# Kernel tuning notes

Hardware: AMD Instinct MI355X
Metric: run time of the kernel (lower is better)

## Reference

```python
import jax, jax.numpy as jnp
from jax import lax
import numpy as np

DIM = 768
HEADS = 8
DH = DIM // HEADS          # 96
M = DIM // 2               # 384 landmarks
PINV_ITERS = 6
RES_K = 33                 # residual depthwise conv kernel
EPS_LN = 1e-5


def layernorm(x, w, b):
    mu = jnp.mean(x, axis=-1, keepdims=True)
    var = jnp.mean((x - mu) ** 2, axis=-1, keepdims=True)
    return (x - mu) * lax.rsqrt(var + EPS_LN) * w + b


def conv1d_same(x, w, b):
    # x: [B, C, N], w: [O, I, K]
    k = w.shape[-1]
    y = lax.conv_general_dilated(x, w, (1,), [(k // 2, k // 2)],
                                 dimension_numbers=('NCH', 'OIH', 'NCH'))
    return y + b[None, :, None]


def moore_penrose_pinv(x, iters=PINV_ITERS):
    # x: [..., m, m]
    abs_x = jnp.abs(x)
    col = jnp.max(abs_x.sum(axis=-1))
    row = jnp.max(abs_x.sum(axis=-2))
    z = jnp.swapaxes(x, -1, -2) / (col * row)
    I = jnp.eye(x.shape[-1], dtype=x.dtype)
    for _ in range(iters):
        xz = x @ z
        z = 0.25 * z @ (13 * I - xz @ (15 * I - xz @ (7 * I - xz)))
    return z


def nystrom_attention(x, qkv_w, out_w, out_b, res_conv_w):
    # x: [B, N, DIM]; N divisible by M here, so no padding branch.
    b, n, _ = x.shape
    qkv = x @ qkv_w.T                                   # [B, N, 3*DIM]
    q, k, v = jnp.split(qkv, 3, axis=-1)
    def heads(t):
        return t.reshape(b, n, HEADS, DH).transpose(0, 2, 1, 3)  # [B,H,N,Dh]
    q, k, v = heads(q), heads(k), heads(v)
    q = q * (DH ** -0.5)

    l = n // M
    q_l = q.reshape(b, HEADS, M, l, DH).mean(axis=3)    # [B,H,M,Dh]
    k_l = k.reshape(b, HEADS, M, l, DH).mean(axis=3)

    sim1 = jnp.einsum('bhnd,bhmd->bhnm', q, k_l)        # [B,H,N,M]
    sim2 = jnp.einsum('bhid,bhjd->bhij', q_l, k_l)      # [B,H,M,M]
    sim3 = jnp.einsum('bhmd,bhnd->bhmn', q_l, k)        # [B,H,M,N]
    attn1 = jax.nn.softmax(sim1, axis=-1)
    attn2 = jax.nn.softmax(sim2, axis=-1)
    attn3 = jax.nn.softmax(sim3, axis=-1)

    attn2_inv = moore_penrose_pinv(attn2)
    out = attn1 @ (attn2_inv @ (attn3 @ v))             # [B,H,N,Dh]

    # residual depthwise conv along sequence, per head: kernel (33,1), groups=HEADS
    res = lax.conv_general_dilated(v, res_conv_w, (1, 1),
                                   [(RES_K // 2, RES_K // 2), (0, 0)],
                                   dimension_numbers=('NCHW', 'OIHW', 'NCHW'),
                                   feature_group_count=HEADS)
    out = out + res
    out = out.transpose(0, 2, 1, 3).reshape(b, n, DIM)
    return out @ out_w.T + out_b


def setup_inputs() -> dict:
    key = jax.random.key(0)
    ks = jax.random.split(key, 16)
    B, N = 2, 3840
    s = 0.02
    return {
        'x': jax.random.normal(ks[0], (B, N, DIM), jnp.float32),
        'conv1_w': jax.random.normal(ks[1], (DIM, DIM, 3), jnp.float32) * s,
        'conv1_b': jnp.zeros((DIM,), jnp.float32),
        'conv2_w': jax.random.normal(ks[2], (DIM, DIM, 5), jnp.float32) * s,
        'conv2_b': jnp.zeros((DIM,), jnp.float32),
        'conv3_w': jax.random.normal(ks[3], (DIM, DIM, 7), jnp.float32) * s,
        'conv3_b': jnp.zeros((DIM,), jnp.float32),
        'norm_w': jnp.ones((DIM,), jnp.float32),
        'norm_b': jnp.zeros((DIM,), jnp.float32),
        'tnorm_w': jnp.ones((DIM,), jnp.float32),
        'tnorm_b': jnp.zeros((DIM,), jnp.float32),
        'qkv_w': jax.random.normal(ks[4], (3 * DIM, DIM), jnp.float32) * s,
        'out_w': jax.random.normal(ks[5], (DIM, DIM), jnp.float32) * s,
        'out_b': jnp.zeros((DIM,), jnp.float32),
        'res_conv_w': jax.random.normal(ks[6], (HEADS, 1, RES_K, 1), jnp.float32) * s,
    }


def reference(x, conv1_w, conv1_b, conv2_w, conv2_b, conv3_w, conv3_b,
              norm_w, norm_b, tnorm_w, tnorm_b, qkv_w, out_w, out_b, res_conv_w):
    inp = x.transpose(0, 2, 1)                              # [B, C, N]
    o1 = jax.nn.relu(layernorm(conv1d_same(inp, conv1_w, conv1_b).transpose(0, 2, 1), norm_w, norm_b))
    o2 = jax.nn.relu(layernorm(conv1d_same(inp, conv2_w, conv2_b).transpose(0, 2, 1), norm_w, norm_b))
    o3 = jax.nn.relu(layernorm(conv1d_same(inp, conv3_w, conv3_b).transpose(0, 2, 1), norm_w, norm_b))
    out = o1 + o2 + o3 + x
    # TransLayer: x + attn(norm(x))  (dropout is identity at inference)
    out = out + nystrom_attention(layernorm(out, tnorm_w, tnorm_b),
                                  qkv_w, out_w, out_b, res_conv_w)
    return layernorm(out, norm_w, norm_b)
```

## Files before the change

### kernel.cpp

```cpp
#include <hip/hip_runtime.h>

#define SEQN 3840
#define BATCH 2
#define DIMC 768
#define NH 8
#define DHD 96
#define ML 384
#define LW 10
#define BHN 16
#define ROWS (BATCH*SEQN)
#define PADX 4
#define XPADN (SEQN + 2*PADX)
#define NCOL3 (3*DIMC)
#define KD7 (7*DIMC)

static const int BND = BATCH*SEQN*DIMC;
static const int MD  = BHN*ML*DHD;
static const int MM_ = BHN*ML*ML;

__device__ __forceinline__ unsigned short f2bf(float f) {
    unsigned int u = __float_as_uint(f);
    u = (u + 0x7FFF + ((u >> 16) & 1)) >> 16;
    return (unsigned short)u;
}
__device__ __forceinline__ float bf2f(unsigned short s) {
    return __uint_as_float(((unsigned int)s) << 16);
}
__device__ __forceinline__ unsigned short f2h(float f) {
    _Float16 h = (_Float16)f;
    return *(unsigned short*)&h;
}
__device__ __forceinline__ float h2f(unsigned short u) {
    _Float16 h = *(_Float16*)&u;
    return (float)h;
}

__device__ __forceinline__ float wave_sum(float v) {
#pragma unroll
    for (int m = 32; m; m >>= 1) v += __shfl_xor(v, m, 64);
    return v;
}
__device__ __forceinline__ float wave_max(float v) {
#pragma unroll
    for (int m = 32; m; m >>= 1) v = fmaxf(v, __shfl_xor(v, m, 64));
    return v;
}

typedef short bf16x8 __attribute__((ext_vector_type(8)));
typedef float f32x4 __attribute__((ext_vector_type(4)));
#define ROWP 40

__global__ __launch_bounds__(256) void mgemm_k(
    const unsigned short* __restrict__ A, int lda, long long sA,
    const unsigned short* __restrict__ Bm, int ldb, long long sB,
    int Mr, int Nc, int Kd, float alpha, int conv_k,
    int epi, float* __restrict__ Cf, long long sC, int ldc,
    unsigned short* __restrict__ Cb, const float* __restrict__ bias,
    unsigned short* __restrict__ Qo, unsigned short* __restrict__ Ko,
    unsigned short* __restrict__ Vo)
{
    __shared__ unsigned short As[128*ROWP] __attribute__((aligned(16)));
    __shared__ unsigned short Bs[128*ROWP] __attribute__((aligned(16)));
    const int bz = blockIdx.z;
    const long long aoff = (long long)bz * sA, boff = (long long)bz * sB;
    const long long coff = (long long)bz * sC;
    const int i0 = blockIdx.y * 128, j0 = blockIdx.x * 128;
    const int tid = threadIdx.x;
    const int w = tid >> 6, l = tid & 63;
    const int wr = (w >> 1) << 6, wc = (w & 1) << 6;
    const int lr = l & 15, lk = l >> 4;
    const int khalf = conv_k >> 1;

    f32x4 acc[4][4] = {};

    for (int k0 = 0; k0 < Kd; k0 += 32) {
#pragma unroll
        for (int pass = 0; pass < 2; ++pass) {
            const int flat = tid + pass * 256;
            const int row = flat >> 2, seg = (flat & 3) << 3;
            long long ga;
            if (conv_k) {
                const int gi = i0 + row;
                const int b = gi / SEQN, n = gi - b * SEQN;
                const int tap = k0 / DIMC, c = k0 - tap * DIMC;
                ga = ((long long)(b * XPADN + n + tap + PADX - khalf)) * DIMC + c + seg;
            } else {
                ga = aoff + (long long)(i0 + row) * lda + k0 + seg;
            }
            *(uint4*)&As[row * ROWP + seg] = *(const uint4*)&A[ga];
        }
#pragma unroll
        for (int pass = 0; pass < 2; ++pass) {
            const int flat = tid + pass * 256;
            const int row = flat >> 2, seg = (flat & 3) << 3;
            const int gj = j0 + row;
            uint4 v;
            if (gj < Nc) v = *(const uint4*)&Bm[boff + (long long)gj * ldb + k0 + seg];
            else { v.x = v.y = v.z = v.w = 0u; }
            *(uint4*)&Bs[row * ROWP + seg] = v;
        }
        __syncthreads();
        bf16x8 af[4], bfv[4];
#pragma unroll
        for (int fi = 0; fi < 4; ++fi)
            af[fi] = *(const bf16x8*)&As[(wr + fi * 16 + lr) * ROWP + lk * 8];
#pragma unroll
        for (int fj = 0; fj < 4; ++fj)
            bfv[fj] = *(const bf16x8*)&Bs[(wc + fj * 16 + lr) * ROWP + lk * 8];
#pragma unroll
        for (int fi = 0; fi < 4; ++fi)
#pragma unroll
            for (int fj = 0; fj < 4; ++fj)
                acc[fi][fj] = __builtin_amdgcn_mfma_f32_16x16x32_bf16(
                    af[fi], bfv[fj], acc[fi][fj], 0, 0, 0);
        __syncthreads();
    }
#pragma unroll
    for (int fi = 0; fi < 4; ++fi) {
#pragma unroll
        for (int fj = 0; fj < 4; ++fj) {
            const int col = j0 + wc + fj * 16 + lr;
            if (col >= Nc) continue;
#pragma unroll
            for (int r = 0; r < 4; ++r) {
                const int row = i0 + wr + fi * 16 + lk * 4 + r;
                float v = acc[fi][fj][r] * alpha;
                if (epi == 0) {
                    Cf[coff + (long long)row * ldc + col] = v;
                } else if (epi == 1) {
                    const long long ix = coff + (long long)row * ldc + col;
                    Cf[ix] = Cf[ix] + v + bias[col];
                } else if (epi == 4) {
                    Cb[coff + (long long)row * ldc + col] = f2h(v);
                } else {
                    const int which = col / DIMC;
                    const int c = col - which * DIMC;
                    const int h = c / DHD, d = c - h * DHD;
                    const int b = row / SEQN, n = row - b * SEQN;
                    const long long o = (((long long)(b * NH + h)) * SEQN + n) * DHD + d;
                    if (which == 0)      Qo[o] = f2bf(v * 0.10206207261596575f);
                    else if (which == 1) Ko[o] = f2bf(v);
                    else                 Vo[o] = f2bf(v);
                }
            }
        }
    }
}

template<int BMODE>
__global__ __launch_bounds__(256) void mgemm64_k(
    const unsigned short* __restrict__ A, int lda, long long sA,
    const unsigned short* __restrict__ Bm, int ldb, long long sB,
    int Mr, int Nc, int Kd, float alpha, int bdiag, float bda, int ksplit,
    int epi, float* __restrict__ Cf, long long sC, int ldc,
    unsigned short* __restrict__ Cb)
{
    __shared__ unsigned short As[64*ROWP] __attribute__((aligned(16)));
    __shared__ unsigned short Bs[64*ROWP] __attribute__((aligned(16)));
    const int bz = blockIdx.z / ksplit;
    const int kch = blockIdx.z - bz * ksplit;
    const long long aoff = (long long)bz * sA, boff = (long long)bz * sB;
    const long long coff = (long long)bz * sC;
    const int i0 = blockIdx.y * 64, j0 = blockIdx.x * 64;
    const int tid = threadIdx.x;
    const int w = tid >> 6, l = tid & 63;
    const int lr = l & 15, lk = l >> 4;
    const int klen = Kd / ksplit;
    const int kbeg = kch * klen, kend = kbeg + klen;

    f32x4 acc[4] = {};

    for (int k0 = kbeg; k0 < kend; k0 += 32) {
        {
            const int row = tid >> 2, seg = (tid & 3) << 3;
            *(uint4*)&As[row*ROWP+seg] =
                *(const uint4*)&A[aoff + (long long)(i0+row)*lda + k0 + seg];
        }
        if (BMODE == 0) {
            const int row = tid >> 2, seg = (tid & 3) << 3;
            const int gj = j0 + row;
            uint4 v;
            if (gj < Nc) v = *(const uint4*)&Bm[boff + (long long)gj*ldb + k0 + seg];
            else { v.x=v.y=v.z=v.w=0u; }
            *(uint4*)&Bs[row*ROWP+seg] = v;
        } else {
            const int kk = tid >> 3, j8 = (tid & 7) << 3;
            const int gk = k0 + kk, gj0 = j0 + j8;
            unsigned short buf[8];
            if (gj0 + 8 <= Nc) {
                *(uint4*)&buf[0] = *(const uint4*)&Bm[boff + (long long)gk*ldb + gj0];
                if (bdiag) {
#pragma unroll
                    for (int u = 0; u < 8; ++u) {
                        float v = ((gk == gj0+u) ? bda : 0.f) - bf2f(buf[u]);
                        buf[u] = f2bf(v);
                    }
                }
            } else {
#pragma unroll
                for (int u = 0; u < 8; ++u) buf[u] = 0;
            }
#pragma unroll
            for (int u = 0; u < 8; ++u) Bs[(j8+u)*ROWP + kk] = buf[u];
        }
        __syncthreads();
        bf16x8 af = *(const bf16x8*)&As[(w*16+lr)*ROWP + lk*8];
        bf16x8 b0 = *(const bf16x8*)&Bs[(lr)*ROWP + lk*8];
        bf16x8 b1 = *(const bf16x8*)&Bs[(16+lr)*ROWP + lk*8];
        bf16x8 b2 = *(const bf16x8*)&Bs[(32+lr)*ROWP + lk*8];
        bf16x8 b3 = *(const bf16x8*)&Bs[(48+lr)*ROWP + lk*8];
        acc[0] = __builtin_amdgcn_mfma_f32_16x16x32_bf16(af, b0, acc[0], 0,0,0);
        acc[1] = __builtin_amdgcn_mfma_f32_16x16x32_bf16(af, b1, acc[1], 0,0,0);
        acc[2] = __builtin_amdgcn_mfma_f32_16x16x32_bf16(af, b2, acc[2], 0,0,0);
        acc[3] = __builtin_amdgcn_mfma_f32_16x16x32_bf16(af, b3, acc[3], 0,0,0);
        __syncthreads();
    }
#pragma unroll
    for (int fj = 0; fj < 4; ++fj) {
        const int col = j0 + fj*16 + lr;
        if (col >= Nc) continue;
#pragma unroll
        for (int r = 0; r < 4; ++r) {
            const int row = i0 + w*16 + lk*4 + r;
            float v = acc[fj][r] * alpha;
            if (epi == 0)      Cf[coff + (long long)row*ldc + col] = v;
            else if (epi == 2) Cb[coff + (long long)row*ldc + col] = f2bf(v);
            else               atomicAdd(&Cf[coff + (long long)row*ldc + col], v);
        }
    }
}

template<int NV>
__global__ __launch_bounds__(256) void softmax_h2b(unsigned short* __restrict__ data, int W)
{
    __shared__ float red[4];
    const long long r = blockIdx.x;
    unsigned short* row = data + r * (long long)W;
    const int t = threadIdx.x, lane = t & 63, wid = t >> 6;
    float v[NV];
    float mx = -3.4e38f;
#pragma unroll
    for (int i = 0; i < NV; ++i) {
        const int j = t + i * 256;
        float f = -3.4e38f;
        if (j < W) f = h2f(row[j]);
        v[i] = f;
        mx = fmaxf(mx, f);
    }
    mx = wave_max(mx);
    if (lane == 0) red[wid] = mx;
    __syncthreads();
    mx = fmaxf(fmaxf(red[0], red[1]), fmaxf(red[2], red[3]));
    __syncthreads();
    float s = 0.f;
#pragma unroll
    for (int i = 0; i < NV; ++i) {
        v[i] = __expf(v[i] - mx);
        s += v[i];
    }
    s = wave_sum(s);
    if (lane == 0) red[wid] = s;
    __syncthreads();
    s = red[0] + red[1] + red[2] + red[3];
    const float inv = 1.f / s;
#pragma unroll
    for (int i = 0; i < NV; ++i) {
        const int j = t + i * 256;
        if (j < W) row[j] = f2bf(v[i] * inv);
    }
}

__global__ __launch_bounds__(256) void ln_kernel(
    const float* __restrict__ in, const float* __restrict__ w,
    const float* __restrict__ b, float* __restrict__ outf,
    unsigned short* __restrict__ outb)
{
    __shared__ float red[4];
    const long long r = blockIdx.x;
    const float* row = in + r * DIMC;
    const int t = threadIdx.x, lane = t & 63, wid = t >> 6;
    float x0 = row[t], x1 = row[t+256], x2 = row[t+512];
    float s = wave_sum(x0 + x1 + x2);
    if (lane == 0) red[wid] = s;
    __syncthreads();
    float mu = (red[0]+red[1]+red[2]+red[3]) * (1.f/DIMC);
    __syncthreads();
    float d0 = x0-mu, d1 = x1-mu, d2 = x2-mu;
    float q = wave_sum(d0*d0 + d1*d1 + d2*d2);
    if (lane == 0) red[wid] = q;
    __syncthreads();
    float rs = rsqrtf((red[0]+red[1]+red[2]+red[3]) * (1.f/DIMC) + 1e-5f);
    float v0 = d0*rs*w[t]     + b[t];
    float v1 = d1*rs*w[t+256] + b[t+256];
    float v2 = d2*rs*w[t+512] + b[t+512];
    if (outf) {
        float* o = outf + r * DIMC;
        o[t] = v0; o[t+256] = v1; o[t+512] = v2;
    }
    if (outb) {
        unsigned short* o = outb + r * DIMC;
        o[t] = f2bf(v0); o[t+256] = f2bf(v1); o[t+512] = f2bf(v2);
    }
}

__global__ __launch_bounds__(256) void ln_relu_add3_kernel(
    const unsigned short* __restrict__ Y16,
    const float* __restrict__ cb0, const float* __restrict__ cb1,
    const float* __restrict__ cb2,
    const float* __restrict__ w, const float* __restrict__ b,
    const float* __restrict__ xin, float* __restrict__ acc)
{
    __shared__ float red[4];
    const long long r = blockIdx.x;
    const unsigned short* row = Y16 + r * NCOL3;
    const int t = threadIdx.x, lane = t & 63, wid = t >> 6;
    const float* xr = xin + r * DIMC;
    float o0 = xr[t], o1 = xr[t+256], o2 = xr[t+512];
    const float* cbs[3] = {cb0, cb1, cb2};
#pragma unroll
    for (int s = 0; s < 3; ++s) {
        const float* cb = cbs[s];
        float x0 = h2f(row[s*DIMC + t])     + cb[t];
        float x1 = h2f(row[s*DIMC + t+256]) + cb[t+256];
        float x2 = h2f(row[s*DIMC + t+512]) + cb[t+512];
        float su = wave_sum(x0 + x1 + x2);
        __syncthreads();
        if (lane == 0) red[wid] = su;
        __syncthreads();
        float mu = (red[0]+red[1]+red[2]+red[3]) * (1.f/DIMC);
        float d0 = x0-mu, d1 = x1-mu, d2 = x2-mu;
        float q = wave_sum(d0*d0 + d1*d1 + d2*d2);
        __syncthreads();
        if (lane == 0) red[wid] = q;
        __syncthreads();
        float rs = rsqrtf((red[0]+red[1]+red[2]+red[3]) * (1.f/DIMC) + 1e-5f);
        o0 += fmaxf(d0*rs*w[t]     + b[t],     0.f);
        o1 += fmaxf(d1*rs*w[t+256] + b[t+256], 0.f);
        o2 += fmaxf(d2*rs*w[t+512] + b[t+512], 0.f);
    }
    float* ar = acc + r * DIMC;
    ar[t] = o0; ar[t+256] = o1; ar[t+512] = o2;
}

__global__ __launch_bounds__(256) void softmax_rows(float* __restrict__ data, int W)
{
    __shared__ float red[4];
    const long long r = blockIdx.x;
    float* row = data + r * (long long)W;
    const int t = threadIdx.x, lane = t & 63, wid = t >> 6;
    float mx = -3.4e38f;
    for (int j = t; j < W; j += 256) mx = fmaxf(mx, row[j]);
    mx = wave_max(mx);
    if (lane == 0) red[wid] = mx;
    __syncthreads();
    mx = fmaxf(fmaxf(red[0], red[1]), fmaxf(red[2], red[3]));
    __syncthreads();
    float s = 0.f;
    for (int j = t; j < W; j += 256) s += __expf(row[j] - mx);
    s = wave_sum(s);
    if (lane == 0) red[wid] = s;
    __syncthreads();
    s = red[0]+red[1]+red[2]+red[3];
    const float inv = 1.f / s;
    for (int j = t; j < W; j += 256) row[j] = __expf(row[j] - mx) * inv;
}

__global__ void pad_x_kernel(const float* __restrict__ x, unsigned short* __restrict__ xp)
{
    int i = blockIdx.x * 256 + threadIdx.x;
    if (i >= BATCH * XPADN * (DIMC/4)) return;
    int e = i * 4;
    int c = e % DIMC; int rr = e / DIMC; int pr = rr % XPADN; int b = rr / XPADN;
    int n = pr - PADX;
    ushort4 o;
    if (n < 0 || n >= SEQN) { o.x = o.y = o.z = o.w = 0; }
    else {
        float4 v = *(const float4*)&x[((long long)(b * SEQN + n)) * DIMC + c];
        o.x = f2bf(v.x); o.y = f2bf(v.y); o.z = f2bf(v.z); o.w = f2bf(v.w);
    }
    *(ushort4*)&xp[e] = o;
}

__global__ void transpose_w7_kernel(const float* __restrict__ W,
                                    unsigned short* __restrict__ WT, int K, int branch)
{
    int idx = blockIdx.x * 256 + threadIdx.x;
    if (idx >= DIMC * 7 * DIMC) return;
    int i = idx % DIMC; int rem = idx / DIMC; int t = rem % 7; int o = rem / 7;
    int k = t - (3 - (K >> 1));
    float v = (k >= 0 && k < K) ? W[((long long)o * DIMC + i) * K + k] : 0.f;
    WT[((long long)(branch * DIMC + o)) * KD7 + t * DIMC + i] = f2bf(v);
}

__global__ void cvt_bf16_kernel(const float* __restrict__ src,
                                unsigned short* __restrict__ dst, int n4)
{
    int i = blockIdx.x * 256 + threadIdx.x;
    if (i >= n4) return;
    float4 v = ((const float4*)src)[i];
    ushort4 o; o.x = f2bf(v.x); o.y = f2bf(v.y); o.z = f2bf(v.z); o.w = f2bf(v.w);
    ((ushort4*)dst)[i] = o;
}

__global__ void zero_f32_kernel(float* __restrict__ p, int n)
{
    int i = blockIdx.x * 256 + threadIdx.x;
    if (i < n) p[i] = 0.f;
}

__global__ void landmark_kernel(const unsigned short* __restrict__ src,
                                unsigned short* __restrict__ dstb)
{
    int idx = blockIdx.x * 256 + threadIdx.x;
    if (idx >= MD) return;
    int d = idx % DHD; int rem = idx / DHD; int m = rem % ML; int bh = rem / ML;
    const unsigned short* p = src + ((long long)bh * SEQN + m * LW) * DHD + d;
    float s = 0.f;
#pragma unroll
    for (int j = 0; j < LW; ++j) s += bf2f(p[(long long)j * DHD]);
    dstb[idx] = f2bf(s * (1.f / LW));
}

__global__ void init_scalars_kernel(float* sc)
{
    if (blockIdx.x == 0 && threadIdx.x < 2) sc[threadIdx.x] = 0.f;
}
__global__ void rowsum_max_kernel(const float* __restrict__ A2, float* sc)
{
    int r = blockIdx.x * 256 + threadIdx.x;
    if (r >= BHN * ML) return;
    const float* row = A2 + (long long)r * ML;
    float s = 0.f;
    for (int j = 0; j < ML; ++j) s += fabsf(row[j]);
    atomicMax((unsigned int*)(sc + 0), __float_as_uint(s));
}
__global__ void colsum_max_kernel(const float* __restrict__ A2, float* sc)
{
    int idx = blockIdx.x * 256 + threadIdx.x;
    if (idx >= BHN * ML) return;
    int j = idx % ML, bh = idx / ML;
    const float* base = A2 + (long long)bh * ML * ML + j;
    float s = 0.f;
    for (int i = 0; i < ML; ++i) s += fabsf(base[(long long)i * ML]);
    atomicMax((unsigned int*)(sc + 1), __float_as_uint(s));
}
__global__ void z0_kernel(const float* __restrict__ A2, const float* __restrict__ sc,
                          unsigned short* __restrict__ Z)
{
    long long idx = (long long)blockIdx.x * 256 + threadIdx.x;
    if (idx >= (long long)MM_) return;
    int j = idx % ML; long long rem = idx / ML; int i = (int)(rem % ML); long long bh = rem / ML;
    float inv = 1.f / (sc[0] * sc[1]);
    Z[idx] = f2bf(A2[(bh * ML + j) * ML + i] * inv);
}

__global__ void resconv_concat_kernel(const unsigned short* __restrict__ V,
                                      const float* __restrict__ RW,
                                      const float* __restrict__ AO,
                                      unsigned short* __restrict__ CT)
{
    int idx = blockIdx.x * 256 + threadIdx.x;
    if (idx >= BND) return;
    int d = idx % DHD; int rem = idx / DHD; int n = rem % SEQN; int bh = rem / SEQN;
    int h = bh % NH, b = bh / NH;
    const unsigned short* vb = V + (long long)bh * SEQN * DHD + d;
    float s = AO[idx];
#pragma unroll
    for (int j = 0; j < 33; ++j) {
        int sn = n + j - 16;
        if (sn >= 0 && sn < SEQN) s += bf2f(vb[(long long)sn * DHD]) * RW[h * 33 + j];
    }
    CT[((long long)(b * SEQN + n)) * DIMC + h * DHD + d] = f2bf(s);
}

__global__ void sentinel_kernel(float* __restrict__ out, int n)
{
    int i = blockIdx.x * 256 + threadIdx.x;
    if (i < n) out[i] = 1.0e6f;
}

extern "C" void kernel_launch(void* const* d_in, const int* in_sizes, int n_in,
                              void* d_out, int out_size, void* d_ws, size_t ws_size,
                              hipStream_t stream)
{
    (void)in_sizes; (void)n_in;
    const float* x    = (const float*)d_in[0];
    const float* c1w  = (const float*)d_in[1];
    const float* c1b  = (const float*)d_in[2];
    const float* c2w  = (const float*)d_in[3];
    const float* c2b  = (const float*)d_in[4];
    const float* c3w  = (const float*)d_in[5];
    const float* c3b  = (const float*)d_in[6];
    const float* nw   = (const float*)d_in[7];
    const float* nb   = (const float*)d_in[8];
    const float* tw   = (const float*)d_in[9];
    const float* tb   = (const float*)d_in[10];
    const float* qkvw = (const float*)d_in[11];
    const float* outw = (const float*)d_in[12];
    const float* outb = (const float*)d_in[13];
    const float* rcw  = (const float*)d_in[14];
    float* out = (float*)d_out;
    float* ws  = (float*)d_ws;

    const int POOLA_F = 7378944;
    const int POOLB_F = 8847360;
    const int POOLC_F = 3538944;
    float* OUT_ACC = ws;
    float* A2f  = OUT_ACC + BND;
    float* QLf  = A2f + MM_;
    float* KLf  = QLf + MD;
    float* Zab  = KLf + MD;
    float* AOf  = Zab + MM_;
    float* poolA = AOf + BND;
    float* poolB = poolA + POOLA_F;
    float* poolC = poolB + POOLB_F;
    float* SC   = poolC + POOLC_F;

    unsigned short* Xpad   = (unsigned short*)poolA;
    unsigned short* Tbf    = Xpad;
    unsigned short* WTbf7  = (unsigned short*)A2f;
    unsigned short* CONVY16= (unsigned short*)poolB;
    unsigned short* Qbf    = (unsigned short*)poolB;
    unsigned short* Kbf    = Qbf + BND;
    unsigned short* Vbf    = Kbf + BND;
    unsigned short* CTbf   = Kbf;
    unsigned short* qkvwb  = (unsigned short*)poolC;
    unsigned short* outwb  = qkvwb + 3*DIMC*DIMC;
    unsigned short* A2bf   = outwb + DIMC*DIMC;
    unsigned short* R3bf   = A2bf + MM_;
    unsigned short* QLbf   = R3bf + MD;
    unsigned short* KLbf   = QLbf + MD;
    unsigned short* W2bf   = KLbf + MD;
    unsigned short* XZbf   = (unsigned short*)A2f;
    unsigned short* T1bf   = XZbf + MM_;
    unsigned short* Zabf   = (unsigned short*)Zab;
    unsigned short* Zbbf   = Zabf + MM_;
    unsigned short* Sh     = (unsigned short*)AOf;
    float* AOf2  = A2f;
    float* R3f32 = QLf;

    size_t need_bytes = (size_t)(SC + 16 - ws) * sizeof(float);
    if (ws_size < need_bytes) {
        sentinel_kernel<<<(out_size + 255)/256, 256, 0, stream>>>(out, out_size);
        return;
    }

    auto mg = [&](const unsigned short* A, int lda, long long sA,
                  const unsigned short* Bm, int ldb, long long sB,
                  int Mr, int Nc, int Kd, float alpha, int convk,
                  int epi, float* Cf, long long sC, int ldc, unsigned short* Cb,
                  const float* bias, unsigned short* Qo, unsigned short* Ko,
                  unsigned short* Vo, int batch) {
        dim3 g((Nc + 127) / 128, Mr / 128, batch), blk(256);
        mgemm_k<<<g, blk, 0, stream>>>(A, lda, sA, Bm, ldb, sB, Mr, Nc, Kd,
            alpha, convk, epi, Cf, sC, ldc, Cb, bias, Qo, Ko, Vo);
    };
    auto mg64 = [&](int bmode, const unsigned short* A, int lda, long long sA,
                    const unsigned short* Bm, int ldb, long long sB,
                    int Mr, int Nc, int Kd, float alpha, int bdiag, float bda,
                    int ksplit, int epi, float* Cf, long long sC, int ldc,
                    unsigned short* Cb, int batch) {
        dim3 g((Nc + 63) / 64, Mr / 64, batch * ksplit), blk(256);
        if (bmode == 0)
            mgemm64_k<0><<<g, blk, 0, stream>>>(A, lda, sA, Bm, ldb, sB, Mr, Nc, Kd,
                alpha, bdiag, bda, ksplit, epi, Cf, sC, ldc, Cb);
        else
            mgemm64_k<1><<<g, blk, 0, stream>>>(A, lda, sA, Bm, ldb, sB, Mr, Nc, Kd,
                alpha, bdiag, bda, ksplit, epi, Cf, sC, ldc, Cb);
    };

    const int DD = DIMC * DIMC;
    const long long sMD = (long long)ML*DHD, sMM = (long long)ML*ML,
                    sND = (long long)SEQN*DHD, sMN = (long long)ML*SEQN;
    const int W7N = DIMC * 7 * DIMC;

    pad_x_kernel<<<(BATCH*XPADN*(DIMC/4) + 255)/256, 256, 0, stream>>>(x, Xpad);
    transpose_w7_kernel<<<(W7N + 255)/256, 256, 0, stream>>>(c1w, WTbf7, 3, 0);
    transpose_w7_kernel<<<(W7N + 255)/256, 256, 0, stream>>>(c2w, WTbf7, 5, 1);
    transpose_w7_kernel<<<(W7N + 255)/256, 256, 0, stream>>>(c3w, WTbf7, 7, 2);
    cvt_bf16_kernel<<<(3*DD/4 + 255)/256, 256, 0, stream>>>(qkvw, qkvwb, 3*DD/4);
    cvt_bf16_kernel<<<(DD/4 + 255)/256, 256, 0, stream>>>(outw, outwb, DD/4);

    mg(Xpad, DIMC, 0, WTbf7, KD7, 0, ROWS, NCOL3, KD7,
       1.f, 7, 4, nullptr, 0, NCOL3, CONVY16, nullptr, nullptr, nullptr, nullptr, 1);

    ln_relu_add3_kernel<<<ROWS, 256, 0, stream>>>(CONVY16, c1b, c2b, c3b, nw, nb, x, OUT_ACC);

    ln_kernel<<<ROWS, 256, 0, stream>>>(OUT_ACC, tw, tb, nullptr, Tbf);

    mg(Tbf, DIMC, 0, qkvwb, DIMC, 0, ROWS, 3*DIMC, DIMC,
       1.f, 0, 3, nullptr, 0, 0, nullptr, nullptr, Qbf, Kbf, Vbf, 1);

    landmark_kernel<<<(MD + 255)/256, 256, 0, stream>>>(Qbf, QLbf);
    landmark_kernel<<<(MD + 255)/256, 256, 0, stream>>>(Kbf, KLbf);

    mg64(0, QLbf, DHD, sMD, KLbf, DHD, sMD, ML, ML, DHD,
         1.f, 0, 0.f, 1, 0, A2f, sMM, ML, nullptr, BHN);
    softmax_rows<<<BHN*ML, 256, 0, stream>>>(A2f, ML);

    init_scalars_kernel<<<1, 64, 0, stream>>>(SC);
    rowsum_max_kernel<<<(BHN*ML + 255)/256, 256, 0, stream>>>(A2f, SC);
    colsum_max_kernel<<<(BHN*ML + 255)/256, 256, 0, stream>>>(A2f, SC);
    z0_kernel<<<(MM_ + 255)/256, 256, 0, stream>>>(A2f, SC, Zabf);
    cvt_bf16_kernel<<<(MM_/4 + 255)/256, 256, 0, stream>>>(A2f, A2bf, MM_/4);

    unsigned short* Zc = Zabf; unsigned short* Zn = Zbbf;
    for (int it = 0; it < 6; ++it) {
        mg64(1, A2bf, ML, sMM, Zc,   ML, sMM, ML, ML, ML, 1.f,   0, 0.f,  1, 2,
             nullptr, sMM, ML, XZbf, BHN);
        mg64(1, XZbf, ML, sMM, XZbf, ML, sMM, ML, ML, ML, 1.f,   1, 7.f,  1, 2,
             nullptr, sMM, ML, Zn,   BHN);
        mg64(1, XZbf, ML, sMM, Zn,   ML, sMM, ML, ML, ML, 1.f,   1, 15.f, 1, 2,
             nullptr, sMM, ML, T1bf, BHN);
        mg64(1, Zc,   ML, sMM, T1bf, ML, sMM, ML, ML, ML, 0.25f, 1, 13.f, 1, 2,
             nullptr, sMM, ML, Zn,   BHN);
        unsigned short* t = Zc; Zc = Zn; Zn = t;
    }

    mg(QLbf, DHD, sMD, Kbf, DHD, sND, ML, SEQN, DHD,
       1.f, 0, 4, nullptr, sMN, SEQN, Sh, nullptr, nullptr, nullptr, nullptr, BHN);
    softmax_h2b<15><<<BHN*ML, 256, 0, stream>>>(Sh, SEQN);
    zero_f32_kernel<<<(MD + 255)/256, 256, 0, stream>>>(R3f32, MD);
    mg64(1, Sh, SEQN, sMN, Vbf, DHD, sND, ML, DHD, SEQN,
         1.f, 0, 0.f, 4, 5, R3f32, sMD, DHD, nullptr, BHN);
    cvt_bf16_kernel<<<(MD/4 + 255)/256, 256, 0, stream>>>(R3f32, R3bf, MD/4);

    mg64(1, Zc, ML, sMM, R3bf, DHD, sMD, ML, DHD, ML,
         1.f, 0, 0.f, 1, 2, nullptr, sMD, DHD, W2bf, BHN);

    mg(Qbf, DHD, sND, KLbf, DHD, sMD, SEQN, ML, DHD,
       1.f, 0, 4, nullptr, sMN, ML, Sh, nullptr, nullptr, nullptr, nullptr, BHN);
    softmax_h2b<2><<<BHN*SEQN, 256, 0, stream>>>(Sh, ML);
    mg64(1, Sh, ML, sMN, W2bf, DHD, sMD, SEQN, DHD, ML,
         1.f, 0, 0.f, 1, 0, AOf2, sND, DHD, nullptr, BHN);

    resconv_concat_kernel<<<(BND + 255)/256, 256, 0, stream>>>(Vbf, rcw, AOf2, CTbf);

    mg(CTbf, DIMC, 0, outwb, DIMC, 0, ROWS, DIMC, DIMC,
       1.f, 0, 1, OUT_ACC, 0, DIMC, nullptr, outb, nullptr, nullptr, nullptr, 1);

    ln_kernel<<<ROWS, 256, 0, stream>>>(OUT_ACC, nw, nb, out, nullptr);
}
```

Before: 1.710 ms.

## Load GEMM tiles directly into LDS with XOR-swizzled layout

The bf16 MFMA GEMM now fills its A and B shared-memory tiles with global_load_lds 16-byte direct transfers, instead of loading into registers and then storing to LDS. The padded row stride is replaced by an unpadded 32-element row with an XOR swizzle on the 8-element chunk index, which keeps fragment reads free of bank conflicts. The conv path computes the batch and sequence base once per block, assuming a 128-row tile never crosses a batch boundary. The bounds checks on B rows and output columns are removed, so any GEMM whose column count is not a multiple of 128 (such as a 96-wide head dimension) would read and write out of range.

```diff
diff --git a/kernel.cpp b/kernel.cpp
--- a/kernel.cpp
+++ b/kernel.cpp
@@ -50,6 +50,10 @@
 typedef float f32x4 __attribute__((ext_vector_type(4)));
 #define ROWP 40
 
+#define GLOAD_LDS16(gp, lp) __builtin_amdgcn_global_load_lds( \
+    (const __attribute__((address_space(1))) void*)(gp), \
+    (__attribute__((address_space(3))) void*)(lp), 16, 0, 0)
+
 __global__ __launch_bounds__(256) void mgemm_k(
     const unsigned short* __restrict__ A, int lda, long long sA,
     const unsigned short* __restrict__ Bm, int ldb, long long sB,
@@ -59,8 +63,8 @@
     unsigned short* __restrict__ Qo, unsigned short* __restrict__ Ko,
     unsigned short* __restrict__ Vo)
 {
-    __shared__ unsigned short As[128*ROWP] __attribute__((aligned(16)));
-    __shared__ unsigned short Bs[128*ROWP] __attribute__((aligned(16)));
+    __shared__ unsigned short As[128*32] __attribute__((aligned(16)));
+    __shared__ unsigned short Bs[128*32] __attribute__((aligned(16)));
     const int bz = blockIdx.z;
     const long long aoff = (long long)bz * sA, boff = (long long)bz * sB;
     const long long coff = (long long)bz * sC;
@@ -71,42 +75,40 @@
     const int lr = l & 15, lk = l >> 4;
     const int khalf = conv_k >> 1;
 
+    const int lrow4  = l >> 2;
+    const int lchunk = (l & 3) ^ ((lrow4 >> 1) & 3);
+    const int pcr = lk ^ ((lr >> 1) & 3);
+
+    const int cb_ = conv_k ? (i0 / SEQN) : 0;
+    const int cn0 = conv_k ? (i0 - cb_ * SEQN) : 0;
+
     f32x4 acc[4][4] = {};
 
     for (int k0 = 0; k0 < Kd; k0 += 32) {
 #pragma unroll
-        for (int pass = 0; pass < 2; ++pass) {
-            const int flat = tid + pass * 256;
-            const int row = flat >> 2, seg = (flat & 3) << 3;
+        for (int p = 0; p < 2; ++p) {
+            const int seg = p * 4 + w;
+            const int row = seg * 16 + lrow4;
             long long ga;
             if (conv_k) {
-                const int gi = i0 + row;
-                const int b = gi / SEQN, n = gi - b * SEQN;
                 const int tap = k0 / DIMC, c = k0 - tap * DIMC;
-                ga = ((long long)(b * XPADN + n + tap + PADX - khalf)) * DIMC + c + seg;
+                ga = ((long long)(cb_ * XPADN + cn0 + row + tap + PADX - khalf)) * DIMC
+                     + c + lchunk * 8;
             } else {
-                ga = aoff + (long long)(i0 + row) * lda + k0 + seg;
+                ga = aoff + (long long)(i0 + row) * lda + k0 + lchunk * 8;
             }
-            *(uint4*)&As[row * ROWP + seg] = *(const uint4*)&A[ga];
+            GLOAD_LDS16(A + ga, As + seg * 512);
+            const long long gb = boff + (long long)(j0 + row) * ldb + k0 + lchunk * 8;
+            GLOAD_LDS16(Bm + gb, Bs + seg * 512);
         }
-#pragma unroll
-        for (int pass = 0; pass < 2; ++pass) {
-            const int flat = tid + pass * 256;
-            const int row = flat >> 2, seg = (flat & 3) << 3;
-            const int gj = j0 + row;
-            uint4 v;
-            if (gj < Nc) v = *(const uint4*)&Bm[boff + (long long)gj * ldb + k0 + seg];
-            else { v.x = v.y = v.z = v.w = 0u; }
-            *(uint4*)&Bs[row * ROWP + seg] = v;
-        }
         __syncthreads();
         bf16x8 af[4], bfv[4];
 #pragma unroll
         for (int fi = 0; fi < 4; ++fi)
-            af[fi] = *(const bf16x8*)&As[(wr + fi * 16 + lr) * ROWP + lk * 8];
+            af[fi] = *(const bf16x8*)&As[(wr + fi * 16 + lr) * 32 + pcr * 8];
 #pragma unroll
         for (int fj = 0; fj < 4; ++fj)
-            bfv[fj] = *(const bf16x8*)&Bs[(wc + fj * 16 + lr) * ROWP + lk * 8];
+            bfv[fj] = *(const bf16x8*)&Bs[(wc + fj * 16 + lr) * 32 + pcr * 8];
 #pragma unroll
         for (int fi = 0; fi < 4; ++fi)
 #pragma unroll
@@ -120,7 +122,6 @@
 #pragma unroll
         for (int fj = 0; fj < 4; ++fj) {
             const int col = j0 + wc + fj * 16 + lr;
-            if (col >= Nc) continue;
 #pragma unroll
             for (int r = 0; r < 4; ++r) {
                 const int row = i0 + wr + fi * 16 + lk * 4 + r;
```

Result: faster. 1.503 ms (-12.1%).
